# Kernel tuning notes

Measured on AMD Instinct MI355X. Metric: run time of the kernel, lower is better.

The kernel has to match this reference:

```python
import jax, jax.numpy as jnp
import numpy as np


def _causal_mask(n):
    # pixelSNAIL get_causal_mask: strict lower triangular (pixel i attends to pixels < i)
    return jnp.tril(jnp.ones((n, n), dtype=jnp.float32), k=-1)


def setup_inputs() -> dict:
    key = jax.random.key(0)
    kq, kk, kv = jax.random.split(key, 3)
    B, H, W, C, CM = 32, 32, 32, 128, 256
    return {
        "query": jax.random.normal(kq, (B, H, W, C), dtype=jnp.float32),
        "key": jax.random.normal(kk, (B, H, W, C), dtype=jnp.float32),
        "value": jax.random.normal(kv, (B, H, W, CM), dtype=jnp.float32),
    }


def reference(query, key, value):
    B = query.shape[0]
    C = key.shape[-1]
    CM = value.shape[-1]
    Nk = int(np.prod(key.shape[1:-1]))
    Nq = int(np.prod(query.shape[1:-1]))
    q = query.reshape(B, Nq, C)
    k = key.reshape(B, Nk, C)
    v = value.reshape(B, Nk, CM)
    # raw QK^T (no 1/sqrt(d) scaling in original)
    dot = jnp.einsum('bqc,bkc->bqk', q, k)
    # NON-STANDARD: softmax over full row first, then multiply by strict causal mask
    probs = jax.nn.softmax(dot, axis=-1) * _causal_mask(Nq)[None]
    mixed = jnp.einsum('bqk,bkm->bqm', probs, v)
    return mixed.reshape(query.shape[:-1] + (CM,))
```

## Files before the change

kernel.cpp:

```cpp
#include <hip/hip_runtime.h>


typedef __attribute__((ext_vector_type(8))) short short8;
typedef __attribute__((ext_vector_type(4))) float floatx4;

#define MFMA16(a, b, c) __builtin_amdgcn_mfma_f32_16x16x32_bf16((a), (b), (c), 0, 0, 0)

constexpr int N = 1024, C = 128, CM = 256, BATCH = 32;
constexpr int BM = 64;
constexpr int BN = 32;
constexpr int NT = N / BN;
constexpr int KFRAG = BN * C;
constexpr int VFRAG = BN * CM;
constexpr int PSTR = 40;

__device__ __forceinline__ unsigned short f2bf(float x) {
    unsigned int u = __float_as_uint(x);
    u += 0x7fffu + ((u >> 16) & 1u);
    return (unsigned short)(u >> 16);
}
__device__ __forceinline__ float bf2f(unsigned short h) {
    return __uint_as_float(((unsigned int)h) << 16);
}
__device__ __forceinline__ uint4 pack8(const unsigned short* s) {
    uint4 u;
    u.x = (unsigned)s[0] | ((unsigned)s[1] << 16);
    u.y = (unsigned)s[2] | ((unsigned)s[3] << 16);
    u.z = (unsigned)s[4] | ((unsigned)s[5] << 16);
    u.w = (unsigned)s[6] | ((unsigned)s[7] << 16);
    return u;
}
__device__ __forceinline__ void gl2lds16(const unsigned short* g, unsigned short* l) {
    __builtin_amdgcn_global_load_lds(
        (const __attribute__((address_space(1))) void*)g,
        (__attribute__((address_space(3))) void*)l, 16, 0, 0);
}

__global__ __launch_bounds__(256, 8)
void prep_kernel(const float* __restrict__ kg, const float* __restrict__ vg,
                 unsigned short* __restrict__ khi, unsigned short* __restrict__ klo,
                 unsigned short* __restrict__ vf)
{
    const int tid = threadIdx.x;
    const int tile = blockIdx.x, bat = blockIdx.y;
    const int n0 = tile * BN;
    const float* kb = kg + (size_t)bat * N * C;
    const float* vb = vg + (size_t)bat * N * CM;
    unsigned short* khb = khi + ((size_t)bat * NT + tile) * KFRAG;
    unsigned short* klb = klo + ((size_t)bat * NT + tile) * KFRAG;
    unsigned short* vfb = vf + ((size_t)bat * NT + tile) * VFRAG;

#pragma unroll
    for (int i = 0; i < 2; ++i) {
        int ch = tid + i * 256;
        int r = ch & 15, qd = (ch >> 4) & 3, ks = (ch >> 6) & 3, t = ch >> 8;
        const float* src = kb + (size_t)(n0 + t * 16 + r) * C + ks * 32 + qd * 8;
        float4 a = *(const float4*)src;
        float4 b = *(const float4*)(src + 4);
        float xs[8] = {a.x, a.y, a.z, a.w, b.x, b.y, b.z, b.w};
        unsigned short hi[8], lo[8];
#pragma unroll
        for (int j = 0; j < 8; ++j) {
            unsigned short h = f2bf(xs[j]);
            hi[j] = h;
            lo[j] = f2bf(xs[j] - bf2f(h));
        }
        *(uint4*)(khb + (size_t)ch * 8) = pack8(hi);
        *(uint4*)(klb + (size_t)ch * 8) = pack8(lo);
    }
#pragma unroll
    for (int i = 0; i < 4; ++i) {
        int ch = tid + i * 256;
        int r = ch & 15, qd = (ch >> 4) & 3, ct = ch >> 6;
        const float* src = vb + (size_t)(n0 + qd * 8) * CM + ct * 16 + r;
        unsigned short o[8];
#pragma unroll
        for (int j = 0; j < 8; ++j)
            o[j] = f2bf(src[(size_t)j * CM]);
        *(uint4*)(vfb + (size_t)ch * 8) = pack8(o);
    }
}

__global__ __launch_bounds__(256, 2)
void attn_kernel(const float* __restrict__ qg, float* __restrict__ og,
                 const unsigned short* __restrict__ khi,
                 const unsigned short* __restrict__ klo,
                 const unsigned short* __restrict__ vf)
{
    __shared__ __align__(16) unsigned short sKhi[2][KFRAG];
    __shared__ __align__(16) unsigned short sKlo[2][KFRAG];
    __shared__ __align__(16) unsigned short sV[VFRAG];
    __shared__ __align__(16) unsigned short sP[4 * 16 * PSTR];

    const int tid = threadIdx.x;
    const int w = tid >> 6, ln = tid & 63;
    const int r = ln & 15, qd = ln >> 4;
    const int bat = blockIdx.x;
    const int qt = blockIdx.y;
    const int q0 = qt * BM;

    const float* qb = qg + (size_t)bat * N * C;
    float* ob = og + (size_t)bat * N * CM;
    const unsigned short* khb = khi + (size_t)bat * NT * KFRAG;
    const unsigned short* klb = klo + (size_t)bat * NT * KFRAG;
    const unsigned short* vfb = vf + (size_t)bat * NT * VFRAG;

    short8 qhi[4], qlo[4];
    {
        const float* qr = qb + (size_t)(q0 + w * 16 + r) * C + qd * 8;
#pragma unroll
        for (int ks = 0; ks < 4; ++ks) {
            float4 a = *(const float4*)(qr + ks * 32);
            float4 b = *(const float4*)(qr + ks * 32 + 4);
            float xs[8] = {a.x, a.y, a.z, a.w, b.x, b.y, b.z, b.w};
            short8 h, l;
#pragma unroll
            for (int j = 0; j < 8; ++j) {
                unsigned short hb = f2bf(xs[j]);
                h[j] = (short)hb;
                l[j] = (short)f2bf(xs[j] - bf2f(hb));
            }
            qhi[ks] = h;
            qlo[ks] = l;
        }
    }

    floatx4 oacc[16];
#pragma unroll
    for (int ct = 0; ct < 16; ++ct) oacc[ct] = (floatx4){0.f, 0.f, 0.f, 0.f};
    float lsum[4] = {0.f, 0.f, 0.f, 0.f};
    const int irow = q0 + w * 16 + qd * 4;
    unsigned short* wP = &sP[w * 16 * PSTR];

    gl2lds16(khb + (size_t)tid * 8,         &sKhi[0][tid * 8]);
    gl2lds16(khb + (size_t)(tid + 256) * 8, &sKhi[0][(tid + 256) * 8]);
    gl2lds16(klb + (size_t)tid * 8,         &sKlo[0][tid * 8]);
    gl2lds16(klb + (size_t)(tid + 256) * 8, &sKlo[0][(tid + 256) * 8]);

    for (int tile = 0; tile < NT; ++tile) {
        const bool pvt = (tile <= 2 * qt + 1);
        const int cb = tile & 1;

        if (pvt) {
            const unsigned short* vs = vfb + (size_t)tile * VFRAG;
#pragma unroll
            for (int i = 0; i < 4; ++i)
                gl2lds16(vs + (size_t)(tid + i * 256) * 8, &sV[(tid + i * 256) * 8]);
        }
        if (tile + 1 < NT) {
            const unsigned short* k1 = khb + (size_t)(tile + 1) * KFRAG;
            const unsigned short* l1 = klb + (size_t)(tile + 1) * KFRAG;
            unsigned short* dh = &sKhi[cb ^ 1][0];
            unsigned short* dl = &sKlo[cb ^ 1][0];
            gl2lds16(k1 + (size_t)tid * 8,         dh + tid * 8);
            gl2lds16(k1 + (size_t)(tid + 256) * 8, dh + (tid + 256) * 8);
            gl2lds16(l1 + (size_t)tid * 8,         dl + tid * 8);
            gl2lds16(l1 + (size_t)(tid + 256) * 8, dl + (tid + 256) * 8);
            asm volatile("s_waitcnt vmcnt(4)" ::: "memory");
        } else {
            asm volatile("s_waitcnt vmcnt(0)" ::: "memory");
        }
        asm volatile("s_barrier" ::: "memory");

#pragma unroll
        for (int t = 0; t < 2; ++t) {
            floatx4 a0 = (floatx4){0.f, 0.f, 0.f, 0.f};
            floatx4 a1 = (floatx4){0.f, 0.f, 0.f, 0.f};
            floatx4 a2 = (floatx4){0.f, 0.f, 0.f, 0.f};
#pragma unroll
            for (int ks = 0; ks < 4; ++ks) {
                short8 bh = *(const short8*)(&sKhi[cb][(((t * 4 + ks) * 64) + ln) * 8]);
                short8 bl = *(const short8*)(&sKlo[cb][(((t * 4 + ks) * 64) + ln) * 8]);
                a0 = MFMA16(qhi[ks], bh, a0);
                a1 = MFMA16(qlo[ks], bh, a1);
                a2 = MFMA16(qhi[ks], bl, a2);
            }
            const int jglob = tile * BN + t * 16 + r;
#pragma unroll
            for (int rg = 0; rg < 4; ++rg) {
                float s = a0[rg] + a1[rg] + a2[rg];
                float p = __expf(s - 40.0f);
                lsum[rg] += p;
                if (pvt) {
                    float pm = (jglob < irow + rg) ? p : 0.0f;
                    wP[(qd * 4 + rg) * PSTR + t * 16 + r] = f2bf(pm);
                }
            }
        }

        if (pvt) {
            asm volatile("s_waitcnt lgkmcnt(0)" ::: "memory");
            short8 ap = *(const short8*)(&wP[r * PSTR + qd * 8]);
#pragma unroll
            for (int ct = 0; ct < 16; ++ct) {
                short8 bv = *(const short8*)(&sV[(ct * 64 + ln) * 8]);
                oacc[ct] = MFMA16(ap, bv, oacc[ct]);
            }
        }
        asm volatile("s_barrier" ::: "memory");
    }

#pragma unroll
    for (int rg = 0; rg < 4; ++rg) {
        float v = lsum[rg];
        v += __shfl_xor(v, 1);
        v += __shfl_xor(v, 2);
        v += __shfl_xor(v, 4);
        v += __shfl_xor(v, 8);
        lsum[rg] = v;
    }

#pragma unroll
    for (int rg = 0; rg < 4; ++rg) {
        float inv = 1.0f / lsum[rg];
        float* orow = ob + (size_t)(q0 + w * 16 + qd * 4 + rg) * CM;
#pragma unroll
        for (int ct = 0; ct < 16; ++ct)
            orow[ct * 16 + r] = oacc[ct][rg] * inv;
    }
}

extern "C" void kernel_launch(void* const* d_in, const int* in_sizes, int n_in,
                              void* d_out, int out_size, void* d_ws, size_t ws_size,
                              hipStream_t stream) {
    const float* q = (const float*)d_in[0];
    const float* k = (const float*)d_in[1];
    const float* v = (const float*)d_in[2];
    float* o = (float*)d_out;
    (void)n_in; (void)in_sizes; (void)out_size; (void)ws_size;

    unsigned short* khi = (unsigned short*)d_ws;
    unsigned short* klo = khi + (size_t)BATCH * NT * KFRAG;
    unsigned short* vf  = klo + (size_t)BATCH * NT * KFRAG;

    prep_kernel<<<dim3(NT, BATCH), dim3(256), 0, stream>>>(k, v, khi, klo, vf);
    attn_kernel<<<dim3(BATCH, N / BM), dim3(256), 0, stream>>>(q, o, khi, klo, vf);
}
```

Before: 159.8 us.

## Pair causal query tiles per block and split value columns across blocks

```diff
diff --git a/kernel.cpp b/kernel.cpp
--- a/kernel.cpp
+++ b/kernel.cpp
@@ -7,7 +7,6 @@
 #define MFMA16(a, b, c) __builtin_amdgcn_mfma_f32_16x16x32_bf16((a), (b), (c), 0, 0, 0)
 
 constexpr int N = 1024, C = 128, CM = 256, BATCH = 32;
-constexpr int BM = 64;
 constexpr int BN = 32;
 constexpr int NT = N / BN;
 constexpr int KFRAG = BN * C;
@@ -89,15 +88,15 @@
 {
     __shared__ __align__(16) unsigned short sKhi[2][KFRAG];
     __shared__ __align__(16) unsigned short sKlo[2][KFRAG];
-    __shared__ __align__(16) unsigned short sV[VFRAG];
-    __shared__ __align__(16) unsigned short sP[4 * 16 * PSTR];
+    __shared__ __align__(16) unsigned short sP[8 * 16 * PSTR];
 
     const int tid = threadIdx.x;
     const int w = tid >> 6, ln = tid & 63;
     const int r = ln & 15, qd = ln >> 4;
     const int bat = blockIdx.x;
-    const int qt = blockIdx.y;
-    const int q0 = qt * BM;
+    const int pair = blockIdx.y;
+    const int half = blockIdx.z;
+    const int sa = pair, sb = 15 - pair;
 
     const float* qb = qg + (size_t)bat * N * C;
     float* ob = og + (size_t)bat * N * CM;
@@ -105,9 +104,11 @@
     const unsigned short* klb = klo + (size_t)bat * NT * KFRAG;
     const unsigned short* vfb = vf + (size_t)bat * NT * VFRAG;
 
-    short8 qhi[4], qlo[4];
-    {
-        const float* qr = qb + (size_t)(q0 + w * 16 + r) * C + qd * 8;
+    short8 qAh[4], qAl[4], qBh[4], qBl[4];
+#pragma unroll
+    for (int f = 0; f < 2; ++f) {
+        const int row = (f ? sb : sa) * 64 + w * 16 + r;
+        const float* qr = qb + (size_t)row * C + qd * 8;
 #pragma unroll
         for (int ks = 0; ks < 4; ++ks) {
             float4 a = *(const float4*)(qr + ks * 32);
@@ -120,17 +121,23 @@
                 h[j] = (short)hb;
                 l[j] = (short)f2bf(xs[j] - bf2f(hb));
             }
-            qhi[ks] = h;
-            qlo[ks] = l;
-        }
-    }
-
-    floatx4 oacc[16];
-#pragma unroll
-    for (int ct = 0; ct < 16; ++ct) oacc[ct] = (floatx4){0.f, 0.f, 0.f, 0.f};
-    float lsum[4] = {0.f, 0.f, 0.f, 0.f};
-    const int irow = q0 + w * 16 + qd * 4;
-    unsigned short* wP = &sP[w * 16 * PSTR];
+            if (f) { qBh[ks] = h; qBl[ks] = l; }
+            else   { qAh[ks] = h; qAl[ks] = l; }
+        }
+    }
+
+    floatx4 oaccA[8], oaccB[8];
+#pragma unroll
+    for (int ct = 0; ct < 8; ++ct) {
+        oaccA[ct] = (floatx4){0.f, 0.f, 0.f, 0.f};
+        oaccB[ct] = (floatx4){0.f, 0.f, 0.f, 0.f};
+    }
+    float lsA[4] = {0.f, 0.f, 0.f, 0.f};
+    float lsB[4] = {0.f, 0.f, 0.f, 0.f};
+    const int irA = sa * 64 + w * 16 + qd * 4;
+    const int irB = sb * 64 + w * 16 + qd * 4;
+    unsigned short* wPA = &sP[(w * 2 + 0) * 16 * PSTR];
+    unsigned short* wPB = &sP[(w * 2 + 1) * 16 * PSTR];
 
     gl2lds16(khb + (size_t)tid * 8,         &sKhi[0][tid * 8]);
     gl2lds16(khb + (size_t)(tid + 256) * 8, &sKhi[0][(tid + 256) * 8]);
@@ -138,14 +145,16 @@
     gl2lds16(klb + (size_t)(tid + 256) * 8, &sKlo[0][(tid + 256) * 8]);
 
     for (int tile = 0; tile < NT; ++tile) {
-        const bool pvt = (tile <= 2 * qt + 1);
         const int cb = tile & 1;
-
-        if (pvt) {
+        const bool pvA = (tile <= 2 * sa + 1);
+        const bool pvB = (tile <= 2 * sb + 1);
+
+        short8 vr[8];
+        if (pvB) {
             const unsigned short* vs = vfb + (size_t)tile * VFRAG;
 #pragma unroll
-            for (int i = 0; i < 4; ++i)
-                gl2lds16(vs + (size_t)(tid + i * 256) * 8, &sV[(tid + i * 256) * 8]);
+            for (int ct = 0; ct < 8; ++ct)
+                vr[ct] = *(const short8*)(vs + (size_t)(((half * 8 + ct) * 64) + ln) * 8);
         }
         if (tile + 1 < NT) {
             const unsigned short* k1 = khb + (size_t)(tile + 1) * KFRAG;
@@ -156,7 +165,8 @@
             gl2lds16(k1 + (size_t)(tid + 256) * 8, dh + (tid + 256) * 8);
             gl2lds16(l1 + (size_t)tid * 8,         dl + tid * 8);
             gl2lds16(l1 + (size_t)(tid + 256) * 8, dl + (tid + 256) * 8);
-            asm volatile("s_waitcnt vmcnt(4)" ::: "memory");
+            if (pvB) asm volatile("s_waitcnt vmcnt(12)" ::: "memory");
+            else     asm volatile("s_waitcnt vmcnt(4)" ::: "memory");
         } else {
             asm volatile("s_waitcnt vmcnt(0)" ::: "memory");
         }
@@ -164,37 +174,44 @@
 
 #pragma unroll
         for (int t = 0; t < 2; ++t) {
-            floatx4 a0 = (floatx4){0.f, 0.f, 0.f, 0.f};
-            floatx4 a1 = (floatx4){0.f, 0.f, 0.f, 0.f};
-            floatx4 a2 = (floatx4){0.f, 0.f, 0.f, 0.f};
+            floatx4 aA0 = (floatx4){0.f,0.f,0.f,0.f}, aA1 = aA0, aA2 = aA0;
+            floatx4 aB0 = aA0, aB1 = aA0, aB2 = aA0;
 #pragma unroll
             for (int ks = 0; ks < 4; ++ks) {
                 short8 bh = *(const short8*)(&sKhi[cb][(((t * 4 + ks) * 64) + ln) * 8]);
                 short8 bl = *(const short8*)(&sKlo[cb][(((t * 4 + ks) * 64) + ln) * 8]);
-                a0 = MFMA16(qhi[ks], bh, a0);
-                a1 = MFMA16(qlo[ks], bh, a1);
-                a2 = MFMA16(qhi[ks], bl, a2);
-            }
-            const int jglob = tile * BN + t * 16 + r;
+                aA0 = MFMA16(qAh[ks], bh, aA0);
+                aA1 = MFMA16(qAl[ks], bh, aA1);
+                aA2 = MFMA16(qAh[ks], bl, aA2);
+                aB0 = MFMA16(qBh[ks], bh, aB0);
+                aB1 = MFMA16(qBl[ks], bh, aB1);
+                aB2 = MFMA16(qBh[ks], bl, aB2);
+            }
+            const int jg = tile * BN + t * 16 + r;
 #pragma unroll
             for (int rg = 0; rg < 4; ++rg) {
-                float s = a0[rg] + a1[rg] + a2[rg];
-                float p = __expf(s - 40.0f);
-                lsum[rg] += p;
-                if (pvt) {
-                    float pm = (jglob < irow + rg) ? p : 0.0f;
-                    wP[(qd * 4 + rg) * PSTR + t * 16 + r] = f2bf(pm);
-                }
-            }
-        }
-
-        if (pvt) {
+                float pA = __expf(aA0[rg] + aA1[rg] + aA2[rg] - 40.0f);
+                float pB = __expf(aB0[rg] + aB1[rg] + aB2[rg] - 40.0f);
+                lsA[rg] += pA;
+                lsB[rg] += pB;
+                if (pvA)
+                    wPA[(qd * 4 + rg) * PSTR + t * 16 + r] = f2bf((jg < irA + rg) ? pA : 0.0f);
+                if (pvB)
+                    wPB[(qd * 4 + rg) * PSTR + t * 16 + r] = f2bf((jg < irB + rg) ? pB : 0.0f);
+            }
+        }
+
+        if (pvB) {
             asm volatile("s_waitcnt lgkmcnt(0)" ::: "memory");
-            short8 ap = *(const short8*)(&wP[r * PSTR + qd * 8]);
-#pragma unroll
-            for (int ct = 0; ct < 16; ++ct) {
-                short8 bv = *(const short8*)(&sV[(ct * 64 + ln) * 8]);
-                oacc[ct] = MFMA16(ap, bv, oacc[ct]);
+            short8 apB = *(const short8*)(&wPB[r * PSTR + qd * 8]);
+#pragma unroll
+            for (int ct = 0; ct < 8; ++ct)
+                oaccB[ct] = MFMA16(apB, vr[ct], oaccB[ct]);
+            if (pvA) {
+                short8 apA = *(const short8*)(&wPA[r * PSTR + qd * 8]);
+#pragma unroll
+                for (int ct = 0; ct < 8; ++ct)
+                    oaccA[ct] = MFMA16(apA, vr[ct], oaccA[ct]);
             }
         }
         asm volatile("s_barrier" ::: "memory");
@@ -202,21 +219,25 @@
 
 #pragma unroll
     for (int rg = 0; rg < 4; ++rg) {
-        float v = lsum[rg];
-        v += __shfl_xor(v, 1);
-        v += __shfl_xor(v, 2);
-        v += __shfl_xor(v, 4);
-        v += __shfl_xor(v, 8);
-        lsum[rg] = v;
+        float a = lsA[rg], b = lsB[rg];
+        a += __shfl_xor(a, 1); b += __shfl_xor(b, 1);
+        a += __shfl_xor(a, 2); b += __shfl_xor(b, 2);
+        a += __shfl_xor(a, 4); b += __shfl_xor(b, 4);
+        a += __shfl_xor(a, 8); b += __shfl_xor(b, 8);
+        lsA[rg] = a; lsB[rg] = b;
     }
 
 #pragma unroll
     for (int rg = 0; rg < 4; ++rg) {
-        float inv = 1.0f / lsum[rg];
-        float* orow = ob + (size_t)(q0 + w * 16 + qd * 4 + rg) * CM;
-#pragma unroll
-        for (int ct = 0; ct < 16; ++ct)
-            orow[ct * 16 + r] = oacc[ct][rg] * inv;
+        float invA = 1.0f / lsA[rg];
+        float invB = 1.0f / lsB[rg];
+        float* oA = ob + (size_t)(irA + rg) * CM + half * 128;
+        float* oB = ob + (size_t)(irB + rg) * CM + half * 128;
+#pragma unroll
+        for (int ct = 0; ct < 8; ++ct) {
+            oA[ct * 16 + r] = oaccA[ct][rg] * invA;
+            oB[ct * 16 + r] = oaccB[ct][rg] * invB;
+        }
     }
 }
 
@@ -234,5 +255,5 @@
     unsigned short* vf  = klo + (size_t)BATCH * NT * KFRAG;
 
     prep_kernel<<<dim3(NT, BATCH), dim3(256), 0, stream>>>(k, v, khi, klo, vf);
-    attn_kernel<<<dim3(BATCH, N / BM), dim3(256), 0, stream>>>(q, o, khi, klo, vf);
-}
+    attn_kernel<<<dim3(BATCH, 8, 2), dim3(256), 0, stream>>>(q, o, khi, klo, vf);
+}
```

Result: slower. 176.7 us (+10.6%).
